# Performance work log

Hardware: AMD Instinct MI355X
Metric: run time of the kernel (lower is better)

Reference implementation:

```python
import jax, jax.numpy as jnp
import numpy as np

D_MODEL = 512
N_HEADS = 8
D_HEAD = D_MODEL // N_HEADS
SCALE = 1.0 / np.sqrt(D_MODEL).astype(np.float32)  # source divides by sqrt(d_model), not sqrt(d_head)


def setup_inputs() -> dict:
    key = jax.random.key(0)
    ks = jax.random.split(key, 9)
    B, S = 4, 2048
    std = 1.0 / np.sqrt(D_MODEL).astype(np.float32)
    x = jax.random.normal(ks[0], (B, S, D_MODEL), dtype=jnp.float32)
    Wq = jax.random.normal(ks[1], (D_MODEL, D_MODEL), dtype=jnp.float32) * std
    bq = jnp.zeros((D_MODEL,), jnp.float32)
    Wk = jax.random.normal(ks[2], (D_MODEL, D_MODEL), dtype=jnp.float32) * std
    bk = jnp.zeros((D_MODEL,), jnp.float32)
    Wv = jax.random.normal(ks[3], (D_MODEL, D_MODEL), dtype=jnp.float32) * std
    bv = jnp.zeros((D_MODEL,), jnp.float32)
    Wo = jax.random.normal(ks[4], (D_MODEL, D_MODEL), dtype=jnp.float32) * std
    bo = jnp.zeros((D_MODEL,), jnp.float32)
    return {"x": x, "Wq": Wq, "bq": bq, "Wk": Wk, "bk": bk,
            "Wv": Wv, "bv": bv, "Wo": Wo, "bo": bo}


def reference(x, Wq, bq, Wk, bk, Wv, bv, Wo, bo):
    B, S, _ = x.shape
    # projections -> [B, H, S, Dh]
    def split_heads(t):
        return t.reshape(B, S, N_HEADS, D_HEAD).transpose(0, 2, 1, 3)
    q = split_heads(x @ Wq + bq)
    k = split_heads(x @ Wk + bk)
    v = split_heads(x @ Wv + bv)
    # scores: [B, H, S, S], scaled by 1/sqrt(d_model) as in source
    scores = jnp.einsum('bhqd,bhkd->bhqk', q, k) * SCALE
    weights = jax.nn.softmax(scores, axis=-1)
    # dropout is identity at inference time
    att = jnp.einsum('bhqk,bhkd->bhqd', weights, v)
    att = att.transpose(0, 2, 1, 3).reshape(B, S, D_MODEL)
    return att @ Wo + bo
```

## Files before the change

### kernel.cpp

```cpp
#include <hip/hip_runtime.h>
#include <math.h>

#define BATCH   4
#define S_LEN   2048
#define DMODEL  512
#define NHEADS  8
#define DHEAD   64
#define M_TOT   8192
#define ATT_SCALE 0.04419417382415922f
#define QSCALE (ATT_SCALE * 1.44269504088896f)

using short8  = __attribute__((ext_vector_type(8))) short;
using short4v = __attribute__((ext_vector_type(4))) short;
using floatx4 = __attribute__((ext_vector_type(4))) float;

__device__ __forceinline__ ushort f2bf(float f) {
    union { float f; unsigned u; } x; x.f = f;
    unsigned u = x.u + 0x7FFFu + ((x.u >> 16) & 1u);
    return (ushort)(u >> 16);
}
__device__ __forceinline__ unsigned pk2(float a, float b) {
    return (unsigned)f2bf(a) | ((unsigned)f2bf(b) << 16);
}
__device__ __forceinline__ unsigned pkr2(float a, float b) {
    unsigned ua = __float_as_uint(a) + 0x8000u;
    unsigned ub = __float_as_uint(b) + 0x8000u;
    return __builtin_amdgcn_perm(ub, ua, 0x07060302u);
}

__global__ __launch_bounds__(256) void prep(
    const float* __restrict__ x,
    const float* __restrict__ Wq, const float* __restrict__ Wk,
    const float* __restrict__ Wv, const float* __restrict__ Wo,
    ushort* __restrict__ xb, ushort* __restrict__ WT)
{
    const int bid = blockIdx.x;
    if (bid < 4096) {
        const int i = (bid * 256 + threadIdx.x) * 4;
        float4 f = *(const float4*)(x + i);
        uint2 o; o.x = pk2(f.x, f.y); o.y = pk2(f.z, f.w);
        *(uint2*)(xb + i) = o;
    } else {
        const int rb = bid - 4096;
        const int p  = rb >> 6;
        const int rem = rb & 63;
        const int n  = (rem >> 5) * 256 + threadIdx.x;
        const int k0 = (rem & 31) * 16;
        const float* W = (p == 0) ? Wq : (p == 1) ? Wk : (p == 2) ? Wv : Wo;
        unsigned u[8];
        #pragma unroll
        for (int j = 0; j < 8; ++j) {
            float a = W[(k0 + 2 * j)     * DMODEL + n];
            float b = W[(k0 + 2 * j + 1) * DMODEL + n];
            u[j] = pk2(a, b);
        }
        ushort* dst = WT + ((size_t)p * DMODEL + n) * DMODEL + k0;
        *(uint4*)dst       = *(uint4*)&u[0];
        *(uint4*)(dst + 8) = *(uint4*)&u[4];
    }
}

__global__ __launch_bounds__(256, 4) void qkv_gemm(
    const ushort* __restrict__ xb, const ushort* __restrict__ WT,
    const float* __restrict__ bq, const float* __restrict__ bk, const float* __restrict__ bv,
    ushort* __restrict__ q, ushort* __restrict__ k, ushort* __restrict__ vT)
{
    __shared__ ushort SMEM[128 * 136];
    ushort (*A)[40] = (ushort(*)[40])SMEM;
    ushort (*B)[40] = (ushort(*)[40])(SMEM + 128 * 40);
    ushort (*CT)[136] = (ushort(*)[136])SMEM;

    const int tid = threadIdx.x;
    const int wv  = tid >> 6, lane = tid & 63, l16 = lane & 15, quad = lane >> 4;
    const int m0  = blockIdx.x * 128;
    const int ng0 = blockIdx.y * 128;
    const int p   = ng0 >> 9;
    const int n0  = ng0 & 511;
    const ushort* Wp  = WT + (size_t)p * DMODEL * DMODEL + (size_t)n0 * DMODEL;
    const float* bias = (p == 0) ? bq : (p == 1) ? bk : bv;
    const float scl   = (p == 0) ? QSCALE : 1.0f;

    const int wm = (wv & 1) * 64, wn = (wv >> 1) * 64;
    floatx4 acc[4][4] = {};
    const int ar = tid >> 1, ac = (tid & 1) * 16;

    uint4 pa0, pa1, pb0, pb1;
    pa0 = *(const uint4*)(xb + (size_t)(m0 + ar) * DMODEL + ac);
    pa1 = *(const uint4*)(xb + (size_t)(m0 + ar) * DMODEL + ac + 8);
    pb0 = *(const uint4*)(Wp + (size_t)ar * DMODEL + ac);
    pb1 = *(const uint4*)(Wp + (size_t)ar * DMODEL + ac + 8);

    for (int k0 = 0; k0 < DMODEL; k0 += 32) {
        *(uint4*)&A[ar][ac] = pa0; *(uint4*)&A[ar][ac + 8] = pa1;
        *(uint4*)&B[ar][ac] = pb0; *(uint4*)&B[ar][ac + 8] = pb1;
        __syncthreads();

        if (k0 + 32 < DMODEL) {
            pa0 = *(const uint4*)(xb + (size_t)(m0 + ar) * DMODEL + k0 + 32 + ac);
            pa1 = *(const uint4*)(xb + (size_t)(m0 + ar) * DMODEL + k0 + 32 + ac + 8);
            pb0 = *(const uint4*)(Wp + (size_t)ar * DMODEL + k0 + 32 + ac);
            pb1 = *(const uint4*)(Wp + (size_t)ar * DMODEL + k0 + 32 + ac + 8);
        }

        short8 af[4], bf[4];
        #pragma unroll
        for (int i = 0; i < 4; ++i) af[i] = *(const short8*)&A[wm + i * 16 + l16][quad * 8];
        #pragma unroll
        for (int c = 0; c < 4; ++c) bf[c] = *(const short8*)&B[wn + c * 16 + l16][quad * 8];
        #pragma unroll
        for (int i = 0; i < 4; ++i)
            #pragma unroll
            for (int c = 0; c < 4; ++c)
                acc[i][c] = __builtin_amdgcn_mfma_f32_16x16x32_bf16(af[i], bf[c], acc[i][c], 0, 0, 0);
        __syncthreads();
    }

    if (p < 2) {
        #pragma unroll
        for (int c = 0; c < 4; ++c) {
            const int n = n0 + wn + c * 16 + l16;
            const float bb = bias[n];
            const int h = n >> 6, dh = n & 63;
            #pragma unroll
            for (int i = 0; i < 4; ++i)
                #pragma unroll
                for (int r = 0; r < 4; ++r) {
                    const int m = m0 + wm + i * 16 + quad * 4 + r;
                    const int b = m >> 11, s = m & 2047;
                    const ushort val = f2bf((acc[i][c][r] + bb) * scl);
                    if (p == 0) q[((size_t)(b * NHEADS + h) * S_LEN + s) * DHEAD + dh] = val;
                    else        k[((size_t)(b * NHEADS + h) * S_LEN + s) * DHEAD + dh] = val;
                }
        }
    } else {
        #pragma unroll
        for (int c = 0; c < 4; ++c) {
            const int n = wn + c * 16 + l16;
            const float bb = bias[n0 + n];
            #pragma unroll
            for (int i = 0; i < 4; ++i) {
                uint2 o;
                o.x = pk2(acc[i][c][0] + bb, acc[i][c][1] + bb);
                o.y = pk2(acc[i][c][2] + bb, acc[i][c][3] + bb);
                *(uint2*)&CT[n][wm + i * 16 + quad * 4] = o;
            }
        }
        __syncthreads();
        const int n  = tid >> 1, mh = (tid & 1) * 64;
        const int gn = n0 + n;
        const int h  = gn >> 6, dh = gn & 63;
        const int b  = m0 >> 11, sb = (m0 & 2047) + mh;
        ushort* dst = vT + ((size_t)(b * NHEADS + h) * DHEAD + dh) * S_LEN + sb;
        #pragma unroll
        for (int j = 0; j < 8; ++j)
            *(uint4*)(dst + j * 8) = *(const uint4*)&CT[n][mh + j * 8];
    }
}

__global__ __launch_bounds__(256, 4) void attn(
    const ushort* __restrict__ Q, const ushort* __restrict__ K,
    const ushort* __restrict__ vT,
    float* __restrict__ Opart, float* __restrict__ Lpart, const int KT)
{
    __shared__ ushort Klds[2][64][72];
    __shared__ ushort Vt[2][64][72];

    const int tid = threadIdx.x;
    const int wv  = tid >> 6, lane = tid & 63, l16 = lane & 15, quad = lane >> 4;
    const int q0  = blockIdx.x * 128;
    const int bh  = blockIdx.y;
    const int ck  = blockIdx.z;
    const int kbase = ck * KT;
    const ushort* Qh = Q  + (size_t)bh * S_LEN * DHEAD;
    const ushort* Kh = K  + (size_t)bh * S_LEN * DHEAD;
    const ushort* Vh = vT + (size_t)bh * DHEAD * S_LEN;

    short8 qf[2][2];
    #pragma unroll
    for (int ni = 0; ni < 2; ++ni) {
        const ushort* qrow = Qh + (size_t)(q0 + wv * 32 + ni * 16 + l16) * DHEAD;
        qf[0][ni] = *(const short8*)(qrow + quad * 8);
        qf[1][ni] = *(const short8*)(qrow + 32 + quad * 8);
    }

    floatx4 oacc[4][2] = {};
    float lsum[2] = {0.f, 0.f};

    const int srow = tid >> 2, sc0 = (tid & 3) * 16;
    uint4 ka, kb, va, vb;
    {
        const ushort* Ks = Kh + (size_t)(kbase * 64 + srow) * DHEAD + sc0;
        const ushort* Vs = Vh + (size_t)srow * S_LEN + kbase * 64 + sc0;
        ka = *(const uint4*)Ks; kb = *(const uint4*)(Ks + 8);
        va = *(const uint4*)Vs; vb = *(const uint4*)(Vs + 8);
    }

    for (int kt = 0; kt < KT; ++kt) {
        const int buf = kt & 1;
        *(uint4*)&Klds[buf][srow][sc0] = ka; *(uint4*)&Klds[buf][srow][sc0 + 8] = kb;
        *(uint4*)&Vt[buf][srow][sc0]   = va; *(uint4*)&Vt[buf][srow][sc0 + 8]   = vb;
        __syncthreads();

        if (kt + 1 < KT) {
            const ushort* Ks = Kh + (size_t)((kbase + kt + 1) * 64 + srow) * DHEAD + sc0;
            const ushort* Vs = Vh + (size_t)srow * S_LEN + (kbase + kt + 1) * 64 + sc0;
            ka = *(const uint4*)Ks; kb = *(const uint4*)(Ks + 8);
            va = *(const uint4*)Vs; vb = *(const uint4*)(Vs + 8);
        }

        #pragma unroll
        for (int mi = 0; mi < 4; ++mi) {
            floatx4 s0 = {}, s1 = {};
            #pragma unroll
            for (int s = 0; s < 2; ++s) {
                short8 kf = *(const short8*)&Klds[buf][mi * 16 + l16][s * 32 + quad * 8];
                s0 = __builtin_amdgcn_mfma_f32_16x16x32_bf16(kf, qf[s][0], s0, 0, 0, 0);
                s1 = __builtin_amdgcn_mfma_f32_16x16x32_bf16(kf, qf[s][1], s1, 0, 0, 0);
            }
            short4v vfr[4];
            #pragma unroll
            for (int c = 0; c < 4; ++c)
                vfr[c] = *(const short4v*)&Vt[buf][c * 16 + l16][mi * 16 + quad * 4];

            {
                const float p0 = __builtin_amdgcn_exp2f(s0[0]);
                const float p1 = __builtin_amdgcn_exp2f(s0[1]);
                const float p2 = __builtin_amdgcn_exp2f(s0[2]);
                const float p3 = __builtin_amdgcn_exp2f(s0[3]);
                lsum[0] += (p0 + p1) + (p2 + p3);
                uint2 o; o.x = pkr2(p0, p1); o.y = pkr2(p2, p3);
                short4v pf; *(uint2*)&pf = o;
                #pragma unroll
                for (int c = 0; c < 4; ++c)
                    oacc[c][0] = __builtin_amdgcn_mfma_f32_16x16x16bf16_1k(vfr[c], pf, oacc[c][0], 0, 0, 0);
            }
            {
                const float p0 = __builtin_amdgcn_exp2f(s1[0]);
                const float p1 = __builtin_amdgcn_exp2f(s1[1]);
                const float p2 = __builtin_amdgcn_exp2f(s1[2]);
                const float p3 = __builtin_amdgcn_exp2f(s1[3]);
                lsum[1] += (p0 + p1) + (p2 + p3);
                uint2 o; o.x = pkr2(p0, p1); o.y = pkr2(p2, p3);
                short4v pf; *(uint2*)&pf = o;
                #pragma unroll
                for (int c = 0; c < 4; ++c)
                    oacc[c][1] = __builtin_amdgcn_mfma_f32_16x16x16bf16_1k(vfr[c], pf, oacc[c][1], 0, 0, 0);
            }
        }
    }

    float tot[2];
    #pragma unroll
    for (int ni = 0; ni < 2; ++ni) {
        float t = lsum[ni];
        t += __shfl_xor(t, 16, 64);
        t += __shfl_xor(t, 32, 64);
        tot[ni] = t;
    }

    #pragma unroll
    for (int ni = 0; ni < 2; ++ni) {
        const int qi = q0 + wv * 32 + ni * 16 + l16;
        const size_t row = (size_t)(ck * 32 + bh) * S_LEN + qi;
        if (quad == 0) Lpart[row] = tot[ni];
        #pragma unroll
        for (int mi = 0; mi < 4; ++mi) {
            float4 o = { oacc[mi][ni][0], oacc[mi][ni][1],
                         oacc[mi][ni][2], oacc[mi][ni][3] };
            *(float4*)&Opart[row * DHEAD + mi * 16 + quad * 4] = o;
        }
    }
}

__global__ __launch_bounds__(256, 4) void out_gemm(
    const float* __restrict__ Opart, const float* __restrict__ Lpart,
    const ushort* __restrict__ WoT, const float* __restrict__ bo,
    float* __restrict__ out)
{
    __shared__ ushort A[64][40];
    __shared__ ushort B[128][40];

    const int tid = threadIdx.x;
    const int wv  = tid >> 6, lane = tid & 63, l16 = lane & 15, quad = lane >> 4;
    const int m0 = blockIdx.x * 64;
    const int n0 = blockIdx.y * 128;

    const int ar = tid >> 2, ac = (tid & 3) * 8;
    const int am = m0 + ar, ab = am >> 11, aq = am & 2047;
    float invl[NHEADS];
    #pragma unroll
    for (int h = 0; h < NHEADS; ++h) {
        const size_t rw = (size_t)(ab * NHEADS + h) * S_LEN + aq;
        invl[h] = 1.f / (Lpart[rw] + Lpart[65536 + rw]);
    }
    const int br = tid >> 1, bc = (tid & 1) * 16;

    floatx4 acc[8] = {};

    for (int k0 = 0; k0 < DMODEL; k0 += 32) {
        const int kk = k0 + ac, h = kk >> 6, dh = kk & 63;
        const float* p0 = Opart + ((size_t)(ab * NHEADS + h) * S_LEN + aq) * DHEAD + dh;
        const float* p1 = p0 + (size_t)65536 * DHEAD;
        float4 a0 = *(const float4*)p0,       a1 = *(const float4*)(p0 + 4);
        float4 c0 = *(const float4*)p1,       c1 = *(const float4*)(p1 + 4);
        const float iv = invl[h];
        uint2 u0, u1;
        u0.x = pk2((a0.x + c0.x) * iv, (a0.y + c0.y) * iv);
        u0.y = pk2((a0.z + c0.z) * iv, (a0.w + c0.w) * iv);
        u1.x = pk2((a1.x + c1.x) * iv, (a1.y + c1.y) * iv);
        u1.y = pk2((a1.z + c1.z) * iv, (a1.w + c1.w) * iv);
        *(uint2*)&A[ar][ac]     = u0;
        *(uint2*)&A[ar][ac + 4] = u1;

        uint4 b0 = *(const uint4*)(WoT + (size_t)(n0 + br) * DMODEL + k0 + bc);
        uint4 b1 = *(const uint4*)(WoT + (size_t)(n0 + br) * DMODEL + k0 + bc + 8);
        *(uint4*)&B[br][bc] = b0; *(uint4*)&B[br][bc + 8] = b1;
        __syncthreads();

        short8 af = *(const short8*)&A[wv * 16 + l16][quad * 8];
        #pragma unroll
        for (int c = 0; c < 8; ++c) {
            short8 bf = *(const short8*)&B[c * 16 + l16][quad * 8];
            acc[c] = __builtin_amdgcn_mfma_f32_16x16x32_bf16(af, bf, acc[c], 0, 0, 0);
        }
        __syncthreads();
    }

    #pragma unroll
    for (int c = 0; c < 8; ++c) {
        const int n = n0 + c * 16 + l16;
        const float bb = bo[n];
        #pragma unroll
        for (int r = 0; r < 4; ++r) {
            const int m = m0 + wv * 16 + quad * 4 + r;
            out[(size_t)m * DMODEL + n] = acc[c][r] + bb;
        }
    }
}

extern "C" void kernel_launch(void* const* d_in, const int* in_sizes, int n_in,
                              void* d_out, int out_size, void* d_ws, size_t ws_size,
                              hipStream_t stream)
{
    const float* x  = (const float*)d_in[0];
    const float* Wq = (const float*)d_in[1];
    const float* bq = (const float*)d_in[2];
    const float* Wk = (const float*)d_in[3];
    const float* bk = (const float*)d_in[4];
    const float* Wv = (const float*)d_in[5];
    const float* bv = (const float*)d_in[6];
    const float* Wo = (const float*)d_in[7];
    const float* bo = (const float*)d_in[8];
    float* out = (float*)d_out;

    ushort* ws = (ushort*)d_ws;
    const size_t SZ = (size_t)M_TOT * DMODEL;
    ushort* xb  = ws;
    ushort* WT  = ws + SZ;
    ushort* q   = WT + 4 * (size_t)DMODEL * DMODEL;
    ushort* k   = q + SZ;
    ushort* vT  = k + SZ;
    float*  Opart = (float*)(vT + SZ);
    float*  Lpart = Opart + 2 * (size_t)32 * S_LEN * DHEAD;

    prep<<<4096 + 256, 256, 0, stream>>>(x, Wq, Wk, Wv, Wo, xb, WT);

    qkv_gemm<<<dim3(M_TOT / 128, 3 * DMODEL / 128), 256, 0, stream>>>(
        xb, WT, bq, bk, bv, q, k, vT);

    attn<<<dim3(S_LEN / 128, BATCH * NHEADS, 2), 256, 0, stream>>>(
        q, k, vT, Opart, Lpart, S_LEN / 64 / 2);

    out_gemm<<<dim3(M_TOT / 64, DMODEL / 128), 256, 0, stream>>>(
        Opart, Lpart, WT + 3 * (size_t)DMODEL * DMODEL, bo, out);
}
```

Baseline: 179.9 us.

## Drop split-K attention; normalize and write bf16 output directly in attn

Removes the two-way key split in the attention kernel, so each block walks the full key range and normalizes its own output. The result is written as a bf16 [B,S,D_MODEL] tensor instead of fp32 partial outputs plus row sums. This cuts the fp32 partial traffic and the merge/normalize work in the output GEMM, which now loads bf16 tiles directly. In exchange the attention grid shrinks from 512 to 256 blocks, which may leave the GPU underoccupied and lengthen each block's serial loop.

```diff
diff --git a/kernel.cpp b/kernel.cpp
--- a/kernel.cpp
+++ b/kernel.cpp
@@ -160,7 +160,7 @@
 __global__ __launch_bounds__(256, 4) void attn(
     const ushort* __restrict__ Q, const ushort* __restrict__ K,
     const ushort* __restrict__ vT,
-    float* __restrict__ Opart, float* __restrict__ Lpart, const int KT)
+    ushort* __restrict__ att, const int KT)
 {
     __shared__ ushort Klds[2][64][72];
     __shared__ ushort Vt[2][64][72];
@@ -169,8 +169,6 @@
     const int wv  = tid >> 6, lane = tid & 63, l16 = lane & 15, quad = lane >> 4;
     const int q0  = blockIdx.x * 128;
     const int bh  = blockIdx.y;
-    const int ck  = blockIdx.z;
-    const int kbase = ck * KT;
     const ushort* Qh = Q  + (size_t)bh * S_LEN * DHEAD;
     const ushort* Kh = K  + (size_t)bh * S_LEN * DHEAD;
     const ushort* Vh = vT + (size_t)bh * DHEAD * S_LEN;
@@ -189,8 +187,8 @@
     const int srow = tid >> 2, sc0 = (tid & 3) * 16;
     uint4 ka, kb, va, vb;
     {
-        const ushort* Ks = Kh + (size_t)(kbase * 64 + srow) * DHEAD + sc0;
-        const ushort* Vs = Vh + (size_t)srow * S_LEN + kbase * 64 + sc0;
+        const ushort* Ks = Kh + (size_t)srow * DHEAD + sc0;
+        const ushort* Vs = Vh + (size_t)srow * S_LEN + sc0;
         ka = *(const uint4*)Ks; kb = *(const uint4*)(Ks + 8);
         va = *(const uint4*)Vs; vb = *(const uint4*)(Vs + 8);
     }
@@ -202,8 +200,8 @@
         __syncthreads();
 
         if (kt + 1 < KT) {
-            const ushort* Ks = Kh + (size_t)((kbase + kt + 1) * 64 + srow) * DHEAD + sc0;
-            const ushort* Vs = Vh + (size_t)srow * S_LEN + (kbase + kt + 1) * 64 + sc0;
+            const ushort* Ks = Kh + (size_t)((kt + 1) * 64 + srow) * DHEAD + sc0;
+            const ushort* Vs = Vh + (size_t)srow * S_LEN + (kt + 1) * 64 + sc0;
             ka = *(const uint4*)Ks; kb = *(const uint4*)(Ks + 8);
             va = *(const uint4*)Vs; vb = *(const uint4*)(Vs + 8);
         }
@@ -249,31 +247,32 @@
         }
     }
 
-    float tot[2];
+    float rin[2];
     #pragma unroll
     for (int ni = 0; ni < 2; ++ni) {
         float t = lsum[ni];
         t += __shfl_xor(t, 16, 64);
         t += __shfl_xor(t, 32, 64);
-        tot[ni] = t;
-    }
-
+        rin[ni] = 1.0f / t;
+    }
+
+    const int b = bh >> 3, h = bh & 7;
     #pragma unroll
     for (int ni = 0; ni < 2; ++ni) {
-        const int qi = q0 + wv * 32 + ni * 16 + l16;
-        const size_t row = (size_t)(ck * 32 + bh) * S_LEN + qi;
-        if (quad == 0) Lpart[row] = tot[ni];
-        #pragma unroll
-        for (int mi = 0; mi < 4; ++mi) {
-            float4 o = { oacc[mi][ni][0], oacc[mi][ni][1],
-                         oacc[mi][ni][2], oacc[mi][ni][3] };
-            *(float4*)&Opart[row * DHEAD + mi * 16 + quad * 4] = o;
+        const int qg = q0 + wv * 32 + ni * 16 + l16;
+        ushort* orow = att + ((size_t)(b * S_LEN + qg)) * DMODEL + h * DHEAD + quad * 4;
+        #pragma unroll
+        for (int c = 0; c < 4; ++c) {
+            uint2 o;
+            o.x = pk2(oacc[c][ni][0] * rin[ni], oacc[c][ni][1] * rin[ni]);
+            o.y = pk2(oacc[c][ni][2] * rin[ni], oacc[c][ni][3] * rin[ni]);
+            *(uint2*)(orow + c * 16) = o;
         }
     }
 }
 
 __global__ __launch_bounds__(256, 4) void out_gemm(
-    const float* __restrict__ Opart, const float* __restrict__ Lpart,
+    const ushort* __restrict__ att,
     const ushort* __restrict__ WoT, const float* __restrict__ bo,
     float* __restrict__ out)
 {
@@ -286,32 +285,12 @@
     const int n0 = blockIdx.y * 128;
 
     const int ar = tid >> 2, ac = (tid & 3) * 8;
-    const int am = m0 + ar, ab = am >> 11, aq = am & 2047;
-    float invl[NHEADS];
-    #pragma unroll
-    for (int h = 0; h < NHEADS; ++h) {
-        const size_t rw = (size_t)(ab * NHEADS + h) * S_LEN + aq;
-        invl[h] = 1.f / (Lpart[rw] + Lpart[65536 + rw]);
-    }
     const int br = tid >> 1, bc = (tid & 1) * 16;
 
     floatx4 acc[8] = {};
 
     for (int k0 = 0; k0 < DMODEL; k0 += 32) {
-        const int kk = k0 + ac, h = kk >> 6, dh = kk & 63;
-        const float* p0 = Opart + ((size_t)(ab * NHEADS + h) * S_LEN + aq) * DHEAD + dh;
-        const float* p1 = p0 + (size_t)65536 * DHEAD;
-        float4 a0 = *(const float4*)p0,       a1 = *(const float4*)(p0 + 4);
-        float4 c0 = *(const float4*)p1,       c1 = *(const float4*)(p1 + 4);
-        const float iv = invl[h];
-        uint2 u0, u1;
-        u0.x = pk2((a0.x + c0.x) * iv, (a0.y + c0.y) * iv);
-        u0.y = pk2((a0.z + c0.z) * iv, (a0.w + c0.w) * iv);
-        u1.x = pk2((a1.x + c1.x) * iv, (a1.y + c1.y) * iv);
-        u1.y = pk2((a1.z + c1.z) * iv, (a1.w + c1.w) * iv);
-        *(uint2*)&A[ar][ac]     = u0;
-        *(uint2*)&A[ar][ac + 4] = u1;
-
+        *(uint4*)&A[ar][ac] = *(const uint4*)(att + (size_t)(m0 + ar) * DMODEL + k0 + ac);
         uint4 b0 = *(const uint4*)(WoT + (size_t)(n0 + br) * DMODEL + k0 + bc);
         uint4 b1 = *(const uint4*)(WoT + (size_t)(n0 + br) * DMODEL + k0 + bc + 8);
         *(uint4*)&B[br][bc] = b0; *(uint4*)&B[br][bc + 8] = b1;
@@ -360,17 +339,16 @@
     ushort* q   = WT + 4 * (size_t)DMODEL * DMODEL;
     ushort* k   = q + SZ;
     ushort* vT  = k + SZ;
-    float*  Opart = (float*)(vT + SZ);
-    float*  Lpart = Opart + 2 * (size_t)32 * S_LEN * DHEAD;
+    ushort* att = vT + SZ;
 
     prep<<<4096 + 256, 256, 0, stream>>>(x, Wq, Wk, Wv, Wo, xb, WT);
 
     qkv_gemm<<<dim3(M_TOT / 128, 3 * DMODEL / 128), 256, 0, stream>>>(
         xb, WT, bq, bk, bv, q, k, vT);
 
-    attn<<<dim3(S_LEN / 128, BATCH * NHEADS, 2), 256, 0, stream>>>(
-        q, k, vT, Opart, Lpart, S_LEN / 64 / 2);
+    attn<<<dim3(S_LEN / 128, BATCH * NHEADS), 256, 0, stream>>>(
+        q, k, vT, att, S_LEN / 64);
 
     out_gemm<<<dim3(M_TOT / 64, DMODEL / 128), 256, 0, stream>>>(
-        Opart, Lpart, WT + 3 * (size_t)DMODEL * DMODEL, bo, out);
-}
+        att, WT + 3 * (size_t)DMODEL * DMODEL, bo, out);
+}
```

Result: faster. 174.2 us (-3.2%).
